# Kernel optimization log

Hardware: AMD Instinct MI355X
Metric: run time of the kernel (lower is better)

## Reference

```python
import jax, jax.numpy as jnp
import numpy as np

N_NODES = 100000
N_REL = 4
N_EDGES = 160000  # per relation
IN_F, HID_F, OUT_F = 128, 128, 64


def hetero_layer(x, edges, W, b):
    """Sum over relations of GraphConv (norm='both'): D_in^-1/2 A_r D_out^-1/2 X W_r + b_r."""
    N = x.shape[0]
    out = jnp.zeros((N, W.shape[2]), dtype=x.dtype)
    for r in range(W.shape[0]):  # small fixed relation count
        src = edges[r, 0]
        dst = edges[r, 1]
        ones = jnp.ones(src.shape[0], dtype=x.dtype)
        deg_out = jnp.clip(jax.ops.segment_sum(ones, src, num_segments=N), 1.0)
        deg_in = jnp.clip(jax.ops.segment_sum(ones, dst, num_segments=N), 1.0)
        # scale src features, project (W first since in_feats >= out_feats), gather, scatter-sum
        h = (x * jax.lax.rsqrt(deg_out)[:, None]) @ W[r]
        agg = jax.ops.segment_sum(h[src], dst, num_segments=N)
        out = out + agg * jax.lax.rsqrt(deg_in)[:, None] + b[r]
    return out


def setup_inputs() -> dict:
    key = jax.random.key(0)
    ks = jax.random.split(key, 6)
    x = jax.random.normal(ks[0], (N_NODES, IN_F), dtype=jnp.float32)
    edges = jax.random.randint(ks[1], (N_REL, 2, N_EDGES), 0, N_NODES, dtype=jnp.int32)
    W1 = jax.random.normal(ks[2], (N_REL, IN_F, HID_F), dtype=jnp.float32) * 0.05
    b1 = jnp.zeros((N_REL, HID_F), dtype=jnp.float32)
    W2 = jax.random.normal(ks[3], (N_REL, HID_F, OUT_F), dtype=jnp.float32) * 0.05
    b2 = jnp.zeros((N_REL, OUT_F), dtype=jnp.float32)
    return {"x": x, "edges": edges, "W1": W1, "b1": b1, "W2": W2, "b2": b2}


def reference(x, edges, W1, b1, W2, b2):
    h = jax.nn.relu(hetero_layer(x, edges, W1, b1))
    return hetero_layer(h, edges, W2, b2)
```

## Files before the change

### kernel.cpp

```cpp
#include <hip/hip_runtime.h>
#include <cstddef>
#include <cstdint>

#define NN   100000
#define NR   4
#define NE   160000
#define SCAN_B 1024
#define GEMMB 512

typedef short bf16x8 __attribute__((ext_vector_type(8)));
typedef float f32x4  __attribute__((ext_vector_type(4)));

__device__ __forceinline__ unsigned short f2bf(float f) {
  union { float f; unsigned u; } v; v.f = f;
  unsigned r = v.u + 0x7fffu + ((v.u >> 16) & 1u);
  return (unsigned short)(r >> 16);
}
__device__ __forceinline__ float bf2f(unsigned short h) {
  union { unsigned u; float f; } v; v.u = ((unsigned)h) << 16;
  return v.f;
}

__device__ __forceinline__ void gll16(const unsigned short* g, unsigned short* l) {
  __builtin_amdgcn_global_load_lds(
      (const __attribute__((address_space(1))) void*)g,
      (__attribute__((address_space(3))) void*)l, 16, 0, 0);
}

#define P1_NBLK 9135
__global__ __launch_bounds__(256) void phase1_k(const int* __restrict__ edges,
                                                const float* __restrict__ x,
                                                const float* __restrict__ W1,
                                                const float* __restrict__ W2,
                                                const float* __restrict__ b1,
                                                const float* __restrict__ b2,
                                                int* __restrict__ cnt_out,
                                                int* __restrict__ cnt_in,
                                                unsigned short* __restrict__ xb,
                                                unsigned short* __restrict__ Wt1,
                                                unsigned short* __restrict__ Wt2,
                                                float* __restrict__ bs1,
                                                float* __restrict__ bs2) {
  const int bid = blockIdx.x;
  const int t = threadIdx.x;
  if (bid < 2500) {
    const int r = bid / 625;
    const int e = (bid - r * 625) * 256 + t;
    const int s = edges[(size_t)r * 2 * NE + e];
    const int d = edges[(size_t)r * 2 * NE + NE + e];
    atomicAdd(&cnt_out[(size_t)r * NN + s], 1);
    atomicAdd(&cnt_in[(size_t)r * NN + d], 1);
  } else if (bid < 8750) {
    const int i = (bid - 2500) * 256 + t;
    const float4 a = *(const float4*)&x[(size_t)i * 8];
    const float4 b = *(const float4*)&x[(size_t)i * 8 + 4];
    unsigned short o[8];
    o[0] = f2bf(a.x); o[1] = f2bf(a.y); o[2] = f2bf(a.z); o[3] = f2bf(a.w);
    o[4] = f2bf(b.x); o[5] = f2bf(b.y); o[6] = f2bf(b.z); o[7] = f2bf(b.w);
    *(bf16x8*)&xb[(size_t)i * 8] = *(bf16x8*)o;
  } else if (bid < 9006) {
    const int i = (bid - 8750) * 256 + t;
    const int r = i / (128 * 128);
    const int k = (i / 128) % 128;
    const int n = i % 128;
    Wt1[((size_t)r * 128 + n) * 128 + k] = f2bf(W1[i]);
  } else if (bid < 9134) {
    const int i = (bid - 9006) * 256 + t;
    const int r = i / (128 * 64);
    const int k = (i / 64) % 128;
    const int n = i % 64;
    Wt2[((size_t)r * 64 + n) * 128 + k] = f2bf(W2[i]);
  } else {
    if (t < 128) bs1[t] = b1[t] + b1[128 + t] + b1[256 + t] + b1[384 + t];
    if (t < 64)  bs2[t] = b2[t] + b2[64 + t] + b2[128 + t] + b2[192 + t];
  }
}

__global__ __launch_bounds__(256) void scan1_k(const int* __restrict__ cnt_in,
                                               int* __restrict__ excl,
                                               int* __restrict__ bsum) {
  const int b = blockIdx.x, t = threadIdx.x;
  const int base = b * SCAN_B;
  int v[4]; int tl = 0;
#pragma unroll
  for (int i = 0; i < 4; ++i) {
    const int idx = base + t * 4 + i;
    int c = 0;
    if (idx < NN) {
      c = cnt_in[idx] + cnt_in[NN + idx] + cnt_in[2 * NN + idx] + cnt_in[3 * NN + idx];
    }
    v[i] = c;
    tl += c;
  }
  __shared__ int sm[256];
  sm[t] = tl;
  __syncthreads();
  for (int off = 1; off < 256; off <<= 1) {
    const int x = (t >= off) ? sm[t - off] : 0;
    __syncthreads();
    sm[t] += x;
    __syncthreads();
  }
  const int incl = sm[t];
  int run = incl - tl;
#pragma unroll
  for (int i = 0; i < 4; ++i) {
    const int idx = base + t * 4 + i;
    if (idx < NN) excl[idx] = run;
    run += v[i];
  }
  if (t == 255) bsum[b] = incl;
}

__global__ __launch_bounds__(128) void scan2_k(int* __restrict__ bsum, int nb) {
  const int t = threadIdx.x;
  __shared__ int sm[128];
  const int v = (t < nb) ? bsum[t] : 0;
  sm[t] = v;
  __syncthreads();
  for (int off = 1; off < 128; off <<= 1) {
    const int x = (t >= off) ? sm[t - off] : 0;
    __syncthreads();
    sm[t] += x;
    __syncthreads();
  }
  if (t < nb) bsum[t] = sm[t] - v;
}

__global__ __launch_bounds__(256) void scan3rs_k(const int* __restrict__ cnt,
                                                 float* __restrict__ rs,
                                                 const int* __restrict__ bsum,
                                                 int* __restrict__ row_ptr,
                                                 int* __restrict__ cursor) {
  const int bid = blockIdx.x, t = threadIdx.x;
  if (bid < 3125) {
    const int i = bid * 256 + t;
    rs[i] = rsqrtf(fmaxf((float)cnt[i], 1.0f));
  } else {
    const int i = (bid - 3125) * 256 + t;
    if (i < NN) {
      const int v = cursor[i] + bsum[i / SCAN_B];
      row_ptr[i] = v;
      cursor[i] = v;
    }
    if (i == 0) row_ptr[NN] = NR * NE;
  }
}

template <int NOUT>
__device__ __forceinline__ void gemm_core(const unsigned short* __restrict__ Xb,
                                          const unsigned short* __restrict__ Wtr,
                                          unsigned short* __restrict__ Hr,
                                          int vb, unsigned short (*Xl)[64 * 128]) {
  const int t = threadIdx.x;
  const int wid = t >> 6;
  const int lane = t & 63;
  const int lg = lane >> 4;
  const int lr = lane & 15;

  constexpr int NF = (NOUT == 128) ? 4 : 2;
  const int rbase = (wid & 1) * 32;
  const int cbase = (wid >> 1) * (NOUT / 2);

  bf16x8 bw[NF][4];
#pragma unroll
  for (int nf = 0; nf < NF; ++nf)
#pragma unroll
    for (int ks = 0; ks < 4; ++ks)
      bw[nf][ks] = *(const bf16x8*)&Wtr[(size_t)(cbase + nf * 16 + lr) * 128 + ks * 32 + lg * 8];

  auto stage = [&](int buf, int tile) {
    const int row0 = tile * 64;
#pragma unroll
    for (int i = 0; i < 4; ++i) {
      const int rl = wid * 16 + i * 4 + (lane >> 4);
      int gr = row0 + rl;
      if (gr >= NN) gr = NN - 1;
      const int q = (lane & 15) ^ (rl & 7);
      gll16(&Xb[(size_t)gr * 128 + q * 8], &Xl[buf][rl * 128 + (lane & 15) * 8]);
    }
  };

  const int ntiles = (NN + 63) / 64;
  int tile = vb;
  stage(0, tile);
  __syncthreads();
  int buf = 0;

  for (; tile < ntiles; tile += 128) {
    const int nxt = tile + 128;
    if (nxt < ntiles) stage(buf ^ 1, nxt);

    f32x4 acc[2][NF];
#pragma unroll
    for (int mf = 0; mf < 2; ++mf)
#pragma unroll
      for (int nf = 0; nf < NF; ++nf) acc[mf][nf] = (f32x4){0.f, 0.f, 0.f, 0.f};

#pragma unroll
    for (int ks = 0; ks < 4; ++ks) {
#pragma unroll
      for (int mf = 0; mf < 2; ++mf) {
        const int r = rbase + mf * 16 + lr;
        const bf16x8 a =
            *(const bf16x8*)&Xl[buf][r * 128 + (((ks * 4 + lg) ^ (lr & 7)) << 3)];
#pragma unroll
        for (int nf = 0; nf < NF; ++nf)
          acc[mf][nf] = __builtin_amdgcn_mfma_f32_16x16x32_bf16(a, bw[nf][ks], acc[mf][nf], 0, 0, 0);
      }
    }

    const int row0 = tile * 64;
#pragma unroll
    for (int mf = 0; mf < 2; ++mf) {
#pragma unroll
      for (int i = 0; i < 4; ++i) {
        const int row = row0 + rbase + mf * 16 + lg * 4 + i;
        if (row < NN) {
#pragma unroll
          for (int nf = 0; nf < NF; ++nf)
            Hr[(size_t)row * NOUT + cbase + nf * 16 + lr] = f2bf(acc[mf][nf][i]);
        }
      }
    }
    __syncthreads();
    buf ^= 1;
  }
}

__global__ __launch_bounds__(256, 2) void phaseC_k(const int* __restrict__ edges,
                                                   const unsigned short* __restrict__ xb,
                                                   const unsigned short* __restrict__ Wt1,
                                                   unsigned short* __restrict__ H,
                                                   const float* __restrict__ rs_out,
                                                   const float* __restrict__ rs_in,
                                                   int* __restrict__ cursor,
                                                   int2* __restrict__ csr) {
  __shared__ unsigned short Xl[2][64 * 128];
  const int bid = blockIdx.x;
  if (bid < GEMMB) {
    const int z = bid >> 7;
    gemm_core<128>(xb, Wt1 + (size_t)z * 128 * 128, H + (size_t)z * NN * 128, bid & 127, Xl);
    return;
  }
  const int vb = bid - GEMMB;
  const int r = vb / 625;
  const int e = (vb - r * 625) * 256 + threadIdx.x;
  const int s = edges[(size_t)r * 2 * NE + e];
  const int d = edges[(size_t)r * 2 * NE + NE + e];
  const int pos = atomicAdd(&cursor[d], 1);
  const float w = rs_in[(size_t)r * NN + d] * rs_out[(size_t)r * NN + s];
  csr[pos] = make_int2(r * NN + s, __float_as_int(w));
}

__global__ __launch_bounds__(256, 2) void gemm_dual_k(const unsigned short* __restrict__ Xb,
                                                      const unsigned short* __restrict__ Wt,
                                                      unsigned short* __restrict__ H) {
  __shared__ unsigned short Xl[2][64 * 128];
  const int zp = blockIdx.z;
  const unsigned short* W0 = Wt + (size_t)(2 * zp) * 64 * 128;
  const unsigned short* W1 = Wt + (size_t)(2 * zp + 1) * 64 * 128;
  unsigned short* H0 = H + (size_t)(2 * zp) * NN * 64;
  unsigned short* H1 = H + (size_t)(2 * zp + 1) * NN * 64;

  const int t = threadIdx.x;
  const int wid = t >> 6;
  const int lane = t & 63;
  const int lg = lane >> 4;
  const int lr = lane & 15;

  const int rbase = (wid & 1) * 32;
  const int cbase = (wid >> 1) * 32;

  bf16x8 bw[2][2][4];
#pragma unroll
  for (int nf = 0; nf < 2; ++nf)
#pragma unroll
    for (int ks = 0; ks < 4; ++ks) {
      bw[0][nf][ks] = *(const bf16x8*)&W0[(size_t)(cbase + nf * 16 + lr) * 128 + ks * 32 + lg * 8];
      bw[1][nf][ks] = *(const bf16x8*)&W1[(size_t)(cbase + nf * 16 + lr) * 128 + ks * 32 + lg * 8];
    }

  auto stage = [&](int buf, int tile) {
    const int row0 = tile * 64;
#pragma unroll
    for (int i = 0; i < 4; ++i) {
      const int rl = wid * 16 + i * 4 + (lane >> 4);
      int gr = row0 + rl;
      if (gr >= NN) gr = NN - 1;
      const int q = (lane & 15) ^ (rl & 7);
      gll16(&Xb[(size_t)gr * 128 + q * 8], &Xl[buf][rl * 128 + (lane & 15) * 8]);
    }
  };

  const int ntiles = (NN + 63) / 64;
  int tile = blockIdx.x;
  stage(0, tile);
  __syncthreads();
  int buf = 0;

  for (; tile < ntiles; tile += 128) {
    const int nxt = tile + 128;
    if (nxt < ntiles) stage(buf ^ 1, nxt);

    f32x4 acc[2][2][2];
#pragma unroll
    for (int mf = 0; mf < 2; ++mf)
#pragma unroll
      for (int rel = 0; rel < 2; ++rel)
#pragma unroll
        for (int nf = 0; nf < 2; ++nf) acc[mf][rel][nf] = (f32x4){0.f, 0.f, 0.f, 0.f};

#pragma unroll
    for (int ks = 0; ks < 4; ++ks) {
#pragma unroll
      for (int mf = 0; mf < 2; ++mf) {
        const int r = rbase + mf * 16 + lr;
        const bf16x8 a =
            *(const bf16x8*)&Xl[buf][r * 128 + (((ks * 4 + lg) ^ (lr & 7)) << 3)];
#pragma unroll
        for (int rel = 0; rel < 2; ++rel)
#pragma unroll
          for (int nf = 0; nf < 2; ++nf)
            acc[mf][rel][nf] = __builtin_amdgcn_mfma_f32_16x16x32_bf16(a, bw[rel][nf][ks], acc[mf][rel][nf], 0, 0, 0);
      }
    }

    const int row0 = tile * 64;
#pragma unroll
    for (int mf = 0; mf < 2; ++mf) {
#pragma unroll
      for (int i = 0; i < 4; ++i) {
        const int row = row0 + rbase + mf * 16 + lg * 4 + i;
        if (row < NN) {
#pragma unroll
          for (int nf = 0; nf < 2; ++nf) {
            H0[(size_t)row * 64 + cbase + nf * 16 + lr] = f2bf(acc[mf][0][nf][i]);
            H1[(size_t)row * 64 + cbase + nf * 16 + lr] = f2bf(acc[mf][1][nf][i]);
          }
        }
      }
    }
    __syncthreads();
    buf ^= 1;
  }
}

__global__ __launch_bounds__(256) void gather1_k(const unsigned short* __restrict__ H,
                                                 const int* __restrict__ row_ptr,
                                                 const int2* __restrict__ csr,
                                                 const float* __restrict__ bs1,
                                                 unsigned short* __restrict__ h1b) {
  const int node = blockIdx.x * 4 + (threadIdx.x >> 6);
  const int lane = threadIdx.x & 63;
  if (node >= NN) return;
  const int g  = lane >> 4;
  const int fl = lane & 15;

  float acc[8];
#pragma unroll
  for (int j = 0; j < 8; ++j) acc[j] = 0.f;

  const int beg = row_ptr[node];
  const int end = row_ptr[node + 1];
  for (int e = beg + g; e < end; e += 4) {
    const int2 p = csr[e];
    const float w = __int_as_float(p.y);
    const bf16x8 h = *(const bf16x8*)&H[(size_t)p.x * 128 + fl * 8];
#pragma unroll
    for (int j = 0; j < 8; ++j)
      acc[j] = fmaf(bf2f((unsigned short)h[j]), w, acc[j]);
  }
#pragma unroll
  for (int j = 0; j < 8; ++j) {
    acc[j] += __shfl_xor(acc[j], 16);
    acc[j] += __shfl_xor(acc[j], 32);
  }
  if (g == 0) {
    const float4 c0 = *(const float4*)&bs1[fl * 8];
    const float4 c1 = *(const float4*)&bs1[fl * 8 + 4];
    unsigned short o[8];
    o[0] = f2bf(fmaxf(acc[0] + c0.x, 0.f));
    o[1] = f2bf(fmaxf(acc[1] + c0.y, 0.f));
    o[2] = f2bf(fmaxf(acc[2] + c0.z, 0.f));
    o[3] = f2bf(fmaxf(acc[3] + c0.w, 0.f));
    o[4] = f2bf(fmaxf(acc[4] + c1.x, 0.f));
    o[5] = f2bf(fmaxf(acc[5] + c1.y, 0.f));
    o[6] = f2bf(fmaxf(acc[6] + c1.z, 0.f));
    o[7] = f2bf(fmaxf(acc[7] + c1.w, 0.f));
    *(bf16x8*)&h1b[(size_t)node * 128 + fl * 8] = *(bf16x8*)o;
  }
}

__global__ __launch_bounds__(256) void gather2_k(const unsigned short* __restrict__ H,
                                                 const int* __restrict__ row_ptr,
                                                 const int2* __restrict__ csr,
                                                 const float* __restrict__ bs2,
                                                 float* __restrict__ out) {
  const int node = blockIdx.x * 4 + (threadIdx.x >> 6);
  const int lane = threadIdx.x & 63;
  if (node >= NN) return;
  const int g  = lane >> 3;
  const int fl = lane & 7;

  float acc[8];
#pragma unroll
  for (int j = 0; j < 8; ++j) acc[j] = 0.f;

  const int beg = row_ptr[node];
  const int end = row_ptr[node + 1];
  for (int e = beg + g; e < end; e += 8) {
    const int2 p = csr[e];
    const float w = __int_as_float(p.y);
    const bf16x8 h = *(const bf16x8*)&H[(size_t)p.x * 64 + fl * 8];
#pragma unroll
    for (int j = 0; j < 8; ++j)
      acc[j] = fmaf(bf2f((unsigned short)h[j]), w, acc[j]);
  }
#pragma unroll
  for (int j = 0; j < 8; ++j) {
    acc[j] += __shfl_xor(acc[j], 8);
    acc[j] += __shfl_xor(acc[j], 16);
    acc[j] += __shfl_xor(acc[j], 32);
  }
  if (g == 0) {
    const float4 c0 = *(const float4*)&bs2[fl * 8];
    const float4 c1 = *(const float4*)&bs2[fl * 8 + 4];
    float4 o0, o1;
    o0.x = acc[0] + c0.x; o0.y = acc[1] + c0.y; o0.z = acc[2] + c0.z; o0.w = acc[3] + c0.w;
    o1.x = acc[4] + c1.x; o1.y = acc[5] + c1.y; o1.z = acc[6] + c1.z; o1.w = acc[7] + c1.w;
    *(float4*)&out[(size_t)node * 64 + fl * 8]     = o0;
    *(float4*)&out[(size_t)node * 64 + fl * 8 + 4] = o1;
  }
}

extern "C" void kernel_launch(void* const* d_in, const int* in_sizes, int n_in,
                              void* d_out, int out_size, void* d_ws, size_t ws_size,
                              hipStream_t stream) {
  const float* x     = (const float*)d_in[0];
  const int*   edges = (const int*)d_in[1];
  const float* W1    = (const float*)d_in[2];
  const float* b1    = (const float*)d_in[3];
  const float* W2    = (const float*)d_in[4];
  const float* b2    = (const float*)d_in[5];
  float* out = (float*)d_out;

  unsigned short* xb   = (unsigned short*)d_ws;
  unsigned short* h1b  = xb;
  unsigned short* Hbuf = xb + (size_t)NN * 128;
  unsigned short* Wt1  = Hbuf + (size_t)NR * NN * 128;
  unsigned short* Wt2  = Wt1 + (size_t)NR * 128 * 128;
  float* rs_out = (float*)(Wt2 + (size_t)NR * 64 * 128);
  float* rs_in  = rs_out + (size_t)NR * NN;
  int* cnt_out  = (int*)(rs_in + (size_t)NR * NN);
  int* cnt_in   = cnt_out + (size_t)NR * NN;
  int* row_ptr  = cnt_in + (size_t)NR * NN;
  int* cursor   = row_ptr + (NN + 1);
  int* bsum     = cursor + NN;
  float* bs1    = (float*)(bsum + 128);
  float* bs2    = bs1 + 128;
  int2* csr     = (int2*)(bs2 + 64);

  const int nb = (NN + SCAN_B - 1) / SCAN_B;

  hipMemsetAsync(cnt_out, 0, (size_t)2 * NR * NN * sizeof(int), stream);
  phase1_k<<<P1_NBLK, 256, 0, stream>>>(edges, x, W1, W2, b1, b2,
                                        cnt_out, cnt_in, xb, Wt1, Wt2, bs1, bs2);
  scan1_k<<<nb, 256, 0, stream>>>(cnt_in, cursor , bsum);
  scan2_k<<<1, 128, 0, stream>>>(bsum, nb);
  scan3rs_k<<<3125 + (NN + 255) / 256, 256, 0, stream>>>(cnt_out, rs_out, bsum, row_ptr, cursor);
  phaseC_k<<<GEMMB + 2500, 256, 0, stream>>>(edges, xb, Wt1, Hbuf, rs_out, rs_in, cursor, csr);
  gather1_k<<<(NN + 3) / 4, 256, 0, stream>>>(Hbuf, row_ptr, csr, bs1, h1b);
  gemm_dual_k<<<dim3(128, 1, 2), 256, 0, stream>>>(h1b, Wt2, Hbuf);
  gather2_k<<<(NN + 3) / 4, 256, 0, stream>>>(Hbuf, row_ptr, csr, bs2, out);
}
```

Measured before the change: 222.5 us.

## Move degree counting alongside layer-1 GEMM and fold memset into prep kernel

The hipMemsetAsync of the degree counters is replaced by zeroing blocks inside the prep kernel. The edge-degree atomic counting moves out of the first kernel into the same launch as the layer-1 GEMM, so the GEMM blocks and the counting blocks run concurrently. The CSR fill becomes its own kernel that runs after the scan. This removes one launch and lets the atomic counting hide behind GEMM work, at the cost of an extra separate launch for the fill and possible contention between the two workloads.

```diff
diff --git a/kernel.cpp b/kernel.cpp
--- a/kernel.cpp
+++ b/kernel.cpp
@@ -27,15 +27,14 @@
       (__attribute__((address_space(3))) void*)l, 16, 0, 0);
 }
 
-#define P1_NBLK 9135
-__global__ __launch_bounds__(256) void phase1_k(const int* __restrict__ edges,
-                                                const float* __restrict__ x,
+#define A_ZERO 782
+#define A_NBLK (A_ZERO + 6250 + 256 + 128 + 1)
+__global__ __launch_bounds__(256) void phaseA_k(const float* __restrict__ x,
                                                 const float* __restrict__ W1,
                                                 const float* __restrict__ W2,
                                                 const float* __restrict__ b1,
                                                 const float* __restrict__ b2,
-                                                int* __restrict__ cnt_out,
-                                                int* __restrict__ cnt_in,
+                                                int* __restrict__ cnt,
                                                 unsigned short* __restrict__ xb,
                                                 unsigned short* __restrict__ Wt1,
                                                 unsigned short* __restrict__ Wt2,
@@ -43,29 +42,25 @@
                                                 float* __restrict__ bs2) {
   const int bid = blockIdx.x;
   const int t = threadIdx.x;
-  if (bid < 2500) {
-    const int r = bid / 625;
-    const int e = (bid - r * 625) * 256 + t;
-    const int s = edges[(size_t)r * 2 * NE + e];
-    const int d = edges[(size_t)r * 2 * NE + NE + e];
-    atomicAdd(&cnt_out[(size_t)r * NN + s], 1);
-    atomicAdd(&cnt_in[(size_t)r * NN + d], 1);
-  } else if (bid < 8750) {
-    const int i = (bid - 2500) * 256 + t;
+  if (bid < A_ZERO) {
+    const int i = bid * 256 + t;
+    if (i < 2 * NR * NN / 4) ((int4*)cnt)[i] = make_int4(0, 0, 0, 0);
+  } else if (bid < A_ZERO + 6250) {
+    const int i = (bid - A_ZERO) * 256 + t;
     const float4 a = *(const float4*)&x[(size_t)i * 8];
     const float4 b = *(const float4*)&x[(size_t)i * 8 + 4];
     unsigned short o[8];
     o[0] = f2bf(a.x); o[1] = f2bf(a.y); o[2] = f2bf(a.z); o[3] = f2bf(a.w);
     o[4] = f2bf(b.x); o[5] = f2bf(b.y); o[6] = f2bf(b.z); o[7] = f2bf(b.w);
     *(bf16x8*)&xb[(size_t)i * 8] = *(bf16x8*)o;
-  } else if (bid < 9006) {
-    const int i = (bid - 8750) * 256 + t;
+  } else if (bid < A_ZERO + 6250 + 256) {
+    const int i = (bid - A_ZERO - 6250) * 256 + t;
     const int r = i / (128 * 128);
     const int k = (i / 128) % 128;
     const int n = i % 128;
     Wt1[((size_t)r * 128 + n) * 128 + k] = f2bf(W1[i]);
-  } else if (bid < 9134) {
-    const int i = (bid - 9006) * 256 + t;
+  } else if (bid < A_ZERO + 6250 + 256 + 128) {
+    const int i = (bid - A_ZERO - 6250 - 256) * 256 + t;
     const int r = i / (128 * 64);
     const int k = (i / 64) % 128;
     const int n = i % 64;
@@ -74,6 +69,211 @@
     if (t < 128) bs1[t] = b1[t] + b1[128 + t] + b1[256 + t] + b1[384 + t];
     if (t < 64)  bs2[t] = b2[t] + b2[64 + t] + b2[128 + t] + b2[192 + t];
   }
+}
+
+template <int NOUT>
+__device__ __forceinline__ void gemm_core(const unsigned short* __restrict__ Xb,
+                                          const unsigned short* __restrict__ Wtr,
+                                          unsigned short* __restrict__ Hr,
+                                          int vb, unsigned short (*Xl)[64 * 128]) {
+  const int t = threadIdx.x;
+  const int wid = t >> 6;
+  const int lane = t & 63;
+  const int lg = lane >> 4;
+  const int lr = lane & 15;
+
+  constexpr int NF = (NOUT == 128) ? 4 : 2;
+  const int rbase = (wid & 1) * 32;
+  const int cbase = (wid >> 1) * (NOUT / 2);
+
+  bf16x8 bw[NF][4];
+#pragma unroll
+  for (int nf = 0; nf < NF; ++nf)
+#pragma unroll
+    for (int ks = 0; ks < 4; ++ks)
+      bw[nf][ks] = *(const bf16x8*)&Wtr[(size_t)(cbase + nf * 16 + lr) * 128 + ks * 32 + lg * 8];
+
+  auto stage = [&](int buf, int tile) {
+    const int row0 = tile * 64;
+#pragma unroll
+    for (int i = 0; i < 4; ++i) {
+      const int rl = wid * 16 + i * 4 + (lane >> 4);
+      int gr = row0 + rl;
+      if (gr >= NN) gr = NN - 1;
+      const int q = (lane & 15) ^ (rl & 7);
+      gll16(&Xb[(size_t)gr * 128 + q * 8], &Xl[buf][rl * 128 + (lane & 15) * 8]);
+    }
+  };
+
+  const int ntiles = (NN + 63) / 64;
+  int tile = vb;
+  stage(0, tile);
+  __syncthreads();
+  int buf = 0;
+
+  for (; tile < ntiles; tile += 128) {
+    const int nxt = tile + 128;
+    if (nxt < ntiles) stage(buf ^ 1, nxt);
+
+    f32x4 acc[2][NF];
+#pragma unroll
+    for (int mf = 0; mf < 2; ++mf)
+#pragma unroll
+      for (int nf = 0; nf < NF; ++nf) acc[mf][nf] = (f32x4){0.f, 0.f, 0.f, 0.f};
+
+#pragma unroll
+    for (int ks = 0; ks < 4; ++ks) {
+#pragma unroll
+      for (int mf = 0; mf < 2; ++mf) {
+        const int r = rbase + mf * 16 + lr;
+        const bf16x8 a =
+            *(const bf16x8*)&Xl[buf][r * 128 + (((ks * 4 + lg) ^ (lr & 7)) << 3)];
+#pragma unroll
+        for (int nf = 0; nf < NF; ++nf)
+          acc[mf][nf] = __builtin_amdgcn_mfma_f32_16x16x32_bf16(a, bw[nf][ks], acc[mf][nf], 0, 0, 0);
+      }
+    }
+
+    const int row0 = tile * 64;
+#pragma unroll
+    for (int mf = 0; mf < 2; ++mf) {
+#pragma unroll
+      for (int i = 0; i < 4; ++i) {
+        const int row = row0 + rbase + mf * 16 + lg * 4 + i;
+        if (row < NN) {
+#pragma unroll
+          for (int nf = 0; nf < NF; ++nf)
+            Hr[(size_t)row * NOUT + cbase + nf * 16 + lr] = f2bf(acc[mf][nf][i]);
+        }
+      }
+    }
+    __syncthreads();
+    buf ^= 1;
+  }
+}
+
+__device__ __forceinline__ void gemm_dual_core64(const unsigned short* __restrict__ Xb,
+                                                 const unsigned short* __restrict__ W0,
+                                                 const unsigned short* __restrict__ W1,
+                                                 unsigned short* __restrict__ H0,
+                                                 unsigned short* __restrict__ H1,
+                                                 int vb, unsigned short (*Xl)[64 * 128]) {
+  const int t = threadIdx.x;
+  const int wid = t >> 6;
+  const int lane = t & 63;
+  const int lg = lane >> 4;
+  const int lr = lane & 15;
+
+  const int rbase = (wid & 1) * 32;
+  const int cbase = (wid >> 1) * 32;
+
+  bf16x8 bw[2][2][4];
+#pragma unroll
+  for (int nf = 0; nf < 2; ++nf)
+#pragma unroll
+    for (int ks = 0; ks < 4; ++ks) {
+      bw[0][nf][ks] = *(const bf16x8*)&W0[(size_t)(cbase + nf * 16 + lr) * 128 + ks * 32 + lg * 8];
+      bw[1][nf][ks] = *(const bf16x8*)&W1[(size_t)(cbase + nf * 16 + lr) * 128 + ks * 32 + lg * 8];
+    }
+
+  auto stage = [&](int buf, int tile) {
+    const int row0 = tile * 64;
+#pragma unroll
+    for (int i = 0; i < 4; ++i) {
+      const int rl = wid * 16 + i * 4 + (lane >> 4);
+      int gr = row0 + rl;
+      if (gr >= NN) gr = NN - 1;
+      const int q = (lane & 15) ^ (rl & 7);
+      gll16(&Xb[(size_t)gr * 128 + q * 8], &Xl[buf][rl * 128 + (lane & 15) * 8]);
+    }
+  };
+
+  const int ntiles = (NN + 63) / 64;
+  int tile = vb;
+  stage(0, tile);
+  __syncthreads();
+  int buf = 0;
+
+  for (; tile < ntiles; tile += 128) {
+    const int nxt = tile + 128;
+    if (nxt < ntiles) stage(buf ^ 1, nxt);
+
+    f32x4 acc[2][2][2];
+#pragma unroll
+    for (int mf = 0; mf < 2; ++mf)
+#pragma unroll
+      for (int rel = 0; rel < 2; ++rel)
+#pragma unroll
+        for (int nf = 0; nf < 2; ++nf) acc[mf][rel][nf] = (f32x4){0.f, 0.f, 0.f, 0.f};
+
+#pragma unroll
+    for (int ks = 0; ks < 4; ++ks) {
+#pragma unroll
+      for (int mf = 0; mf < 2; ++mf) {
+        const int r = rbase + mf * 16 + lr;
+        const bf16x8 a =
+            *(const bf16x8*)&Xl[buf][r * 128 + (((ks * 4 + lg) ^ (lr & 7)) << 3)];
+#pragma unroll
+        for (int rel = 0; rel < 2; ++rel)
+#pragma unroll
+          for (int nf = 0; nf < 2; ++nf)
+            acc[mf][rel][nf] = __builtin_amdgcn_mfma_f32_16x16x32_bf16(a, bw[rel][nf][ks], acc[mf][rel][nf], 0, 0, 0);
+      }
+    }
+
+    const int row0 = tile * 64;
+#pragma unroll
+    for (int mf = 0; mf < 2; ++mf) {
+#pragma unroll
+      for (int i = 0; i < 4; ++i) {
+        const int row = row0 + rbase + mf * 16 + lg * 4 + i;
+        if (row < NN) {
+#pragma unroll
+          for (int nf = 0; nf < 2; ++nf) {
+            H0[(size_t)row * 64 + cbase + nf * 16 + lr] = f2bf(acc[mf][0][nf][i]);
+            H1[(size_t)row * 64 + cbase + nf * 16 + lr] = f2bf(acc[mf][1][nf][i]);
+          }
+        }
+      }
+    }
+    __syncthreads();
+    buf ^= 1;
+  }
+}
+
+__global__ __launch_bounds__(256, 2) void phaseB_k(const int* __restrict__ edges,
+                                                   const unsigned short* __restrict__ xb,
+                                                   const unsigned short* __restrict__ Wt1,
+                                                   unsigned short* __restrict__ H,
+                                                   int* __restrict__ cnt_out,
+                                                   int* __restrict__ cnt_in) {
+  __shared__ unsigned short Xl[2][64 * 128];
+  const int bid = blockIdx.x;
+  if (bid < GEMMB) {
+    const int z = bid >> 7;
+    gemm_core<128>(xb, Wt1 + (size_t)z * 128 * 128, H + (size_t)z * NN * 128, bid & 127, Xl);
+    return;
+  }
+  const int idx = bid - GEMMB;
+  const int r = idx / 625;
+  const int e = (idx - r * 625) * 256 + threadIdx.x;
+  const int s = edges[(size_t)r * 2 * NE + e];
+  const int d = edges[(size_t)r * 2 * NE + NE + e];
+  atomicAdd(&cnt_out[(size_t)r * NN + s], 1);
+  atomicAdd(&cnt_in[(size_t)r * NN + d], 1);
+}
+
+__global__ __launch_bounds__(256, 2) void gemm_dual_k(const unsigned short* __restrict__ Xb,
+                                                      const unsigned short* __restrict__ Wt,
+                                                      unsigned short* __restrict__ H) {
+  __shared__ unsigned short Xl[2][64 * 128];
+  const int zp = blockIdx.z;
+  gemm_dual_core64(Xb,
+                   Wt + (size_t)(2 * zp) * 64 * 128,
+                   Wt + (size_t)(2 * zp + 1) * 64 * 128,
+                   H + (size_t)(2 * zp) * NN * 64,
+                   H + (size_t)(2 * zp + 1) * NN * 64,
+                   blockIdx.x, Xl);
 }
 
 __global__ __launch_bounds__(256) void scan1_k(const int* __restrict__ cnt_in,
@@ -147,203 +347,19 @@
   }
 }
 
-template <int NOUT>
-__device__ __forceinline__ void gemm_core(const unsigned short* __restrict__ Xb,
-                                          const unsigned short* __restrict__ Wtr,
-                                          unsigned short* __restrict__ Hr,
-                                          int vb, unsigned short (*Xl)[64 * 128]) {
-  const int t = threadIdx.x;
-  const int wid = t >> 6;
-  const int lane = t & 63;
-  const int lg = lane >> 4;
-  const int lr = lane & 15;
-
-  constexpr int NF = (NOUT == 128) ? 4 : 2;
-  const int rbase = (wid & 1) * 32;
-  const int cbase = (wid >> 1) * (NOUT / 2);
-
-  bf16x8 bw[NF][4];
-#pragma unroll
-  for (int nf = 0; nf < NF; ++nf)
-#pragma unroll
-    for (int ks = 0; ks < 4; ++ks)
-      bw[nf][ks] = *(const bf16x8*)&Wtr[(size_t)(cbase + nf * 16 + lr) * 128 + ks * 32 + lg * 8];
-
-  auto stage = [&](int buf, int tile) {
-    const int row0 = tile * 64;
-#pragma unroll
-    for (int i = 0; i < 4; ++i) {
-      const int rl = wid * 16 + i * 4 + (lane >> 4);
-      int gr = row0 + rl;
-      if (gr >= NN) gr = NN - 1;
-      const int q = (lane & 15) ^ (rl & 7);
-      gll16(&Xb[(size_t)gr * 128 + q * 8], &Xl[buf][rl * 128 + (lane & 15) * 8]);
-    }
-  };
-
-  const int ntiles = (NN + 63) / 64;
-  int tile = vb;
-  stage(0, tile);
-  __syncthreads();
-  int buf = 0;
-
-  for (; tile < ntiles; tile += 128) {
-    const int nxt = tile + 128;
-    if (nxt < ntiles) stage(buf ^ 1, nxt);
-
-    f32x4 acc[2][NF];
-#pragma unroll
-    for (int mf = 0; mf < 2; ++mf)
-#pragma unroll
-      for (int nf = 0; nf < NF; ++nf) acc[mf][nf] = (f32x4){0.f, 0.f, 0.f, 0.f};
-
-#pragma unroll
-    for (int ks = 0; ks < 4; ++ks) {
-#pragma unroll
-      for (int mf = 0; mf < 2; ++mf) {
-        const int r = rbase + mf * 16 + lr;
-        const bf16x8 a =
-            *(const bf16x8*)&Xl[buf][r * 128 + (((ks * 4 + lg) ^ (lr & 7)) << 3)];
-#pragma unroll
-        for (int nf = 0; nf < NF; ++nf)
-          acc[mf][nf] = __builtin_amdgcn_mfma_f32_16x16x32_bf16(a, bw[nf][ks], acc[mf][nf], 0, 0, 0);
-      }
-    }
-
-    const int row0 = tile * 64;
-#pragma unroll
-    for (int mf = 0; mf < 2; ++mf) {
-#pragma unroll
-      for (int i = 0; i < 4; ++i) {
-        const int row = row0 + rbase + mf * 16 + lg * 4 + i;
-        if (row < NN) {
-#pragma unroll
-          for (int nf = 0; nf < NF; ++nf)
-            Hr[(size_t)row * NOUT + cbase + nf * 16 + lr] = f2bf(acc[mf][nf][i]);
-        }
-      }
-    }
-    __syncthreads();
-    buf ^= 1;
-  }
-}
-
-__global__ __launch_bounds__(256, 2) void phaseC_k(const int* __restrict__ edges,
-                                                   const unsigned short* __restrict__ xb,
-                                                   const unsigned short* __restrict__ Wt1,
-                                                   unsigned short* __restrict__ H,
-                                                   const float* __restrict__ rs_out,
-                                                   const float* __restrict__ rs_in,
-                                                   int* __restrict__ cursor,
-                                                   int2* __restrict__ csr) {
-  __shared__ unsigned short Xl[2][64 * 128];
-  const int bid = blockIdx.x;
-  if (bid < GEMMB) {
-    const int z = bid >> 7;
-    gemm_core<128>(xb, Wt1 + (size_t)z * 128 * 128, H + (size_t)z * NN * 128, bid & 127, Xl);
-    return;
-  }
-  const int vb = bid - GEMMB;
-  const int r = vb / 625;
-  const int e = (vb - r * 625) * 256 + threadIdx.x;
+__global__ __launch_bounds__(256) void fill_k(const int* __restrict__ edges,
+                                              const float* __restrict__ rs_out,
+                                              const float* __restrict__ rs_in,
+                                              int* __restrict__ cursor,
+                                              int2* __restrict__ csr) {
+  const int r = blockIdx.y;
+  const int e = blockIdx.x * 256 + threadIdx.x;
+  if (e >= NE) return;
   const int s = edges[(size_t)r * 2 * NE + e];
   const int d = edges[(size_t)r * 2 * NE + NE + e];
   const int pos = atomicAdd(&cursor[d], 1);
   const float w = rs_in[(size_t)r * NN + d] * rs_out[(size_t)r * NN + s];
   csr[pos] = make_int2(r * NN + s, __float_as_int(w));
-}
-
-__global__ __launch_bounds__(256, 2) void gemm_dual_k(const unsigned short* __restrict__ Xb,
-                                                      const unsigned short* __restrict__ Wt,
-                                                      unsigned short* __restrict__ H) {
-  __shared__ unsigned short Xl[2][64 * 128];
-  const int zp = blockIdx.z;
-  const unsigned short* W0 = Wt + (size_t)(2 * zp) * 64 * 128;
-  const unsigned short* W1 = Wt + (size_t)(2 * zp + 1) * 64 * 128;
-  unsigned short* H0 = H + (size_t)(2 * zp) * NN * 64;
-  unsigned short* H1 = H + (size_t)(2 * zp + 1) * NN * 64;
-
-  const int t = threadIdx.x;
-  const int wid = t >> 6;
-  const int lane = t & 63;
-  const int lg = lane >> 4;
-  const int lr = lane & 15;
-
-  const int rbase = (wid & 1) * 32;
-  const int cbase = (wid >> 1) * 32;
-
-  bf16x8 bw[2][2][4];
-#pragma unroll
-  for (int nf = 0; nf < 2; ++nf)
-#pragma unroll
-    for (int ks = 0; ks < 4; ++ks) {
-      bw[0][nf][ks] = *(const bf16x8*)&W0[(size_t)(cbase + nf * 16 + lr) * 128 + ks * 32 + lg * 8];
-      bw[1][nf][ks] = *(const bf16x8*)&W1[(size_t)(cbase + nf * 16 + lr) * 128 + ks * 32 + lg * 8];
-    }
-
-  auto stage = [&](int buf, int tile) {
-    const int row0 = tile * 64;
-#pragma unroll
-    for (int i = 0; i < 4; ++i) {
-      const int rl = wid * 16 + i * 4 + (lane >> 4);
-      int gr = row0 + rl;
-      if (gr >= NN) gr = NN - 1;
-      const int q = (lane & 15) ^ (rl & 7);
-      gll16(&Xb[(size_t)gr * 128 + q * 8], &Xl[buf][rl * 128 + (lane & 15) * 8]);
-    }
-  };
-
-  const int ntiles = (NN + 63) / 64;
-  int tile = blockIdx.x;
-  stage(0, tile);
-  __syncthreads();
-  int buf = 0;
-
-  for (; tile < ntiles; tile += 128) {
-    const int nxt = tile + 128;
-    if (nxt < ntiles) stage(buf ^ 1, nxt);
-
-    f32x4 acc[2][2][2];
-#pragma unroll
-    for (int mf = 0; mf < 2; ++mf)
-#pragma unroll
-      for (int rel = 0; rel < 2; ++rel)
-#pragma unroll
-        for (int nf = 0; nf < 2; ++nf) acc[mf][rel][nf] = (f32x4){0.f, 0.f, 0.f, 0.f};
-
-#pragma unroll
-    for (int ks = 0; ks < 4; ++ks) {
-#pragma unroll
-      for (int mf = 0; mf < 2; ++mf) {
-        const int r = rbase + mf * 16 + lr;
-        const bf16x8 a =
-            *(const bf16x8*)&Xl[buf][r * 128 + (((ks * 4 + lg) ^ (lr & 7)) << 3)];
-#pragma unroll
-        for (int rel = 0; rel < 2; ++rel)
-#pragma unroll
-          for (int nf = 0; nf < 2; ++nf)
-            acc[mf][rel][nf] = __builtin_amdgcn_mfma_f32_16x16x32_bf16(a, bw[rel][nf][ks], acc[mf][rel][nf], 0, 0, 0);
-      }
-    }
-
-    const int row0 = tile * 64;
-#pragma unroll
-    for (int mf = 0; mf < 2; ++mf) {
-#pragma unroll
-      for (int i = 0; i < 4; ++i) {
-        const int row = row0 + rbase + mf * 16 + lg * 4 + i;
-        if (row < NN) {
-#pragma unroll
-          for (int nf = 0; nf < 2; ++nf) {
-            H0[(size_t)row * 64 + cbase + nf * 16 + lr] = f2bf(acc[mf][0][nf][i]);
-            H1[(size_t)row * 64 + cbase + nf * 16 + lr] = f2bf(acc[mf][1][nf][i]);
-          }
-        }
-      }
-    }
-    __syncthreads();
-    buf ^= 1;
-  }
 }
 
 __global__ __launch_bounds__(256) void gather1_k(const unsigned short* __restrict__ H,
@@ -463,13 +479,12 @@
 
   const int nb = (NN + SCAN_B - 1) / SCAN_B;
 
-  hipMemsetAsync(cnt_out, 0, (size_t)2 * NR * NN * sizeof(int), stream);
-  phase1_k<<<P1_NBLK, 256, 0, stream>>>(edges, x, W1, W2, b1, b2,
-                                        cnt_out, cnt_in, xb, Wt1, Wt2, bs1, bs2);
+  phaseA_k<<<A_NBLK, 256, 0, stream>>>(x, W1, W2, b1, b2, cnt_out, xb, Wt1, Wt2, bs1, bs2);
+  phaseB_k<<<GEMMB + 2500, 256, 0, stream>>>(edges, xb, Wt1, Hbuf, cnt_out, cnt_in);
   scan1_k<<<nb, 256, 0, stream>>>(cnt_in, cursor , bsum);
   scan2_k<<<1, 128, 0, stream>>>(bsum, nb);
   scan3rs_k<<<3125 + (NN + 255) / 256, 256, 0, stream>>>(cnt_out, rs_out, bsum, row_ptr, cursor);
-  phaseC_k<<<GEMMB + 2500, 256, 0, stream>>>(edges, xb, Wt1, Hbuf, rs_out, rs_in, cursor, csr);
+  fill_k<<<dim3((NE + 255) / 256, NR), 256, 0, stream>>>(edges, rs_out, rs_in, cursor, csr);
   gather1_k<<<(NN + 3) / 4, 256, 0, stream>>>(Hbuf, row_ptr, csr, bs1, h1b);
   gemm_dual_k<<<dim3(128, 1, 2), 256, 0, stream>>>(h1b, Wt2, Hbuf);
   gather2_k<<<(NN + 3) / 4, 256, 0, stream>>>(Hbuf, row_ptr, csr, bs2, out);
```

Result: faster. 217.1 us (-2.5%).
